# Performance work log

Hardware: AMD Instinct MI355X
Metric: run time of the kernel (lower is better)

The kernel has to match this reference:

```python
import jax, jax.numpy as jnp
import numpy as np

B, L, D, H, NL, FF, W, V = 4, 8192, 256, 4, 4, 1024, 512, 14
DH = D // H


def _ln(x, g, b, eps=1e-5):
    m = jnp.mean(x, axis=-1, keepdims=True)
    v = jnp.mean((x - m) ** 2, axis=-1, keepdims=True)
    return (x - m) / jnp.sqrt(v + eps) * g + b


def setup_inputs() -> dict:
    key = jax.random.key(0)
    ks = jax.random.split(key, 12)
    s = 0.02
    inp = {
        "byte_ids": jax.random.randint(ks[0], (B, L), 0, V, dtype=jnp.int32),
        "embed": jax.random.normal(ks[1], (V, D), jnp.float32) * s,
        "wq": jax.random.normal(ks[2], (NL, D, D), jnp.float32) * s,
        "bq": jnp.zeros((NL, D), jnp.float32),
        "wk": jax.random.normal(ks[3], (NL, D, D), jnp.float32) * s,
        "bk": jnp.zeros((NL, D), jnp.float32),
        "wv": jax.random.normal(ks[4], (NL, D, D), jnp.float32) * s,
        "bv": jnp.zeros((NL, D), jnp.float32),
        "wo": jax.random.normal(ks[5], (NL, D, D), jnp.float32) * s,
        "bo": jnp.zeros((NL, D), jnp.float32),
        "ln1_g": jnp.ones((NL, D), jnp.float32),
        "ln1_b": jnp.zeros((NL, D), jnp.float32),
        "ln2_g": jnp.ones((NL, D), jnp.float32),
        "ln2_b": jnp.zeros((NL, D), jnp.float32),
        "w1": jax.random.normal(ks[6], (NL, D, FF), jnp.float32) * s,
        "b1": jnp.zeros((NL, FF), jnp.float32),
        "w2": jax.random.normal(ks[7], (NL, FF, D), jnp.float32) * s,
        "b2": jnp.zeros((NL, D), jnp.float32),
        "lnf_g": jnp.ones((D,), jnp.float32),
        "lnf_b": jnp.zeros((D,), jnp.float32),
        "head_w": jax.random.normal(ks[8], (D, V), jnp.float32) * s,
    }
    return inp


def _forward(byte_ids, embed, wq, bq, wk, bk, wv, bv, wo, bo,
             ln1_g, ln1_b, ln2_g, ln2_b, w1, b1, w2, b2, lnf_g, lnf_b, head_w):
    x = embed[byte_ids]                      # [B, L, D]
    nb = L // W                              # number of 512-wide blocks
    scale = 1.0 / np.sqrt(DH)
    # ALiBi slopes: 2^(-8h/H) for h = 1..H
    slopes = jnp.exp2(-8.0 * jnp.arange(1, H + 1, dtype=jnp.float32) / H)
    qi = jnp.arange(W)[:, None]
    ki = jnp.arange(2 * W)[None, :]
    dist = (W + qi - ki).astype(jnp.float32)            # i - j for kv window [prev, cur]
    base = (dist >= 0) & (dist <= W)                    # causal sliding window (left=512)
    mask = jnp.broadcast_to(base, (nb, W, 2 * W))
    mask = mask.at[0].set(base & (ki >= W))             # first block has no previous block
    bias = -slopes[:, None, None] * dist                # [H, W, 2W]

    for l in range(NL):
        h = _ln(x, ln1_g[l], ln1_b[l])
        q = (h @ wq[l] + bq[l]).reshape(B, nb, W, H, DH)
        k = (h @ wk[l] + bk[l]).reshape(B, nb, W, H, DH)
        v = (h @ wv[l] + bv[l]).reshape(B, nb, W, H, DH)
        kp = jnp.pad(k, ((0, 0), (1, 0), (0, 0), (0, 0), (0, 0)))[:, :nb]
        vp = jnp.pad(v, ((0, 0), (1, 0), (0, 0), (0, 0), (0, 0)))[:, :nb]
        kk = jnp.concatenate([kp, k], axis=2)           # [B, nb, 2W, H, DH]
        vv = jnp.concatenate([vp, v], axis=2)
        s = jnp.einsum('bnqhd,bnkhd->bhnqk', q, kk) * scale + bias[None, :, None]
        s = jnp.where(mask[None, None], s, -1e9)
        p = jax.nn.softmax(s, axis=-1)                  # [B, H, nb, W, 2W]
        o = jnp.einsum('bhnqk,bnkhd->bnqhd', p, vv).reshape(B, L, D)
        x = x + o @ wo[l] + bo[l]
        h2 = _ln(x, ln2_g[l], ln2_b[l])
        x = x + jax.nn.gelu(h2 @ w1[l] + b1[l]) @ w2[l] + b2[l]
    x = _ln(x, lnf_g, lnf_b)
    return x @ head_w                                   # [B, L, V]


def reference(byte_ids, embed, wq, bq, wk, bk, wv, bv, wo, bo,
              ln1_g, ln1_b, ln2_g, ln2_b, w1, b1, w2, b2, lnf_g, lnf_b, head_w):
    return _forward(byte_ids, embed, wq, bq, wk, bk, wv, bv, wo, bo,
                    ln1_g, ln1_b, ln2_g, ln2_b, w1, b1, w2, b2, lnf_g, lnf_b, head_w)
```

## Files before the change

kernel.cpp:

```cpp
#include <hip/hip_runtime.h>

#define NLAYER 4
#define M_TOK 32768

typedef unsigned short u16;
typedef __bf16 bf16x8 __attribute__((ext_vector_type(8)));
typedef float f32x4 __attribute__((ext_vector_type(4)));

__device__ inline float bf2f(u16 u) {
    union { unsigned int i; float f; } x; x.i = ((unsigned int)u) << 16; return x.f;
}
__device__ inline u16 f2bf(float f) {
    union { float f; unsigned int i; } x; x.f = f;
    return (u16)((x.i + 0x8000u) >> 16);
}
__device__ inline bf16x8 ld_frag(const u16* p) {
    union { uint4 u; bf16x8 b; } c; c.u = *(const uint4*)p; return c.b;
}
__device__ inline unsigned pk2(float a, float b) {
    union { float f; unsigned i; } ua, ub; ua.f = a; ub.f = b;
    return __builtin_amdgcn_perm(ub.i + 0x8000u, ua.i + 0x8000u, 0x07060302u);
}
__device__ inline float gelu_f(float x) {
    float z = 0.7978845608028654f * (x + 0.044715f * x * x * x);
    float t = 1.f - 2.f / (__expf(2.f * z) + 1.f);
    return 0.5f * x * (1.f + t);
}
__device__ inline void gload_lds16(const u16* g, u16* l) {
    __builtin_amdgcn_global_load_lds(
        (const __attribute__((address_space(1))) unsigned int*)g,
        (__attribute__((address_space(3))) unsigned int*)l, 16, 0, 0);
}

#define BAR()   asm volatile("s_barrier" ::: "memory")
#define WAIT4() asm volatile("s_waitcnt vmcnt(4)" ::: "memory")
#define WAIT2() asm volatile("s_waitcnt vmcnt(2)" ::: "memory")
#define WAIT0() asm volatile("s_waitcnt vmcnt(0)" ::: "memory")
#define LGKM0() asm volatile("s_waitcnt lgkmcnt(0)" ::: "memory")

__global__ void sniff_kernel(const u16* __restrict__ raw, int* __restrict__ flag)
{
    if (threadIdx.x == 0 && blockIdx.x == 0) {
        int ok = 1;
        for (int i = 0; i < 32; i++) {
            u16 u = raw[i];
            int e = (u >> 7) & 0xFF;
            if (!(u == 0 || (e >= 90 && e <= 140))) ok = 0;
        }
        *flag = ok;
    }
}

struct IngestArgs { const void* src[20]; int off[21]; };
__global__ __launch_bounds__(256) void ingest_all(
    IngestArgs a, float* __restrict__ dst, const int* __restrict__ flag, int tot)
{
    int gid = blockIdx.x * 256 + threadIdx.x;
    if (gid >= tot) return;
    int lo = 0, hi = 20;
    while (hi - lo > 1) { int mid = (lo + hi) >> 1; if (gid >= a.off[mid]) lo = mid; else hi = mid; }
    int local = gid - a.off[lo];
    if (*flag) dst[gid] = bf2f(((const u16*)a.src[lo])[local]);
    else       dst[gid] = ((const float*)a.src[lo])[local];
}

__global__ __launch_bounds__(256) void pack_qkv(
    const float* __restrict__ wq, const float* __restrict__ wk, const float* __restrict__ wv,
    const float* __restrict__ bq, const float* __restrict__ bk, const float* __restrict__ bv,
    u16* __restrict__ wT, float* __restrict__ bT)
{
    int l = blockIdx.y;
    int idx = blockIdx.x * 256 + threadIdx.x;
    int n = idx >> 8, k = idx & 255;
    const float* w = (n < 256) ? wq : (n < 512) ? wk : wv;
    int nn = n & 255;
    wT[(size_t)l * 768 * 256 + idx] = f2bf(w[(size_t)l * 65536 + k * 256 + nn]);
    if (idx < 768) {
        const float* bb = (idx < 256) ? bq : (idx < 512) ? bk : bv;
        bT[l * 768 + idx] = bb[l * 256 + (idx & 255)];
    }
}

__global__ __launch_bounds__(256) void pack_t(
    const float* __restrict__ src, u16* __restrict__ dst, int R, int C)
{
    int l = blockIdx.y;
    int idx = blockIdx.x * 256 + threadIdx.x;
    int c = idx / R, r = idx % R;
    size_t base = (size_t)l * R * C;
    dst[base + idx] = f2bf(src[base + (size_t)r * C + c]);
}

__global__ __launch_bounds__(256) void embed_ln(
    const int* __restrict__ ids, const float* __restrict__ emb,
    const float* __restrict__ g, const float* __restrict__ b,
    float* __restrict__ x, u16* __restrict__ h)
{
    int t = blockIdx.x * 256 + threadIdx.x;
    int row = t >> 6, c = (t & 63) * 4;
    int id = ids[row];
    float4 e = *(const float4*)(emb + (size_t)id * 256 + c);
    *(float4*)(x + (size_t)row * 256 + c) = e;
    float s = e.x + e.y + e.z + e.w;
    float s2 = e.x * e.x + e.y * e.y + e.z * e.z + e.w * e.w;
    #pragma unroll
    for (int mk = 1; mk < 64; mk <<= 1) {
        s += __shfl_xor(s, mk, 64);
        s2 += __shfl_xor(s2, mk, 64);
    }
    float mean = s * (1.f / 256.f);
    float var = s2 * (1.f / 256.f) - mean * mean;
    float rstd = rsqrtf(var + 1e-5f);
    float4 gg = *(const float4*)(g + c);
    float4 bb = *(const float4*)(b + c);
    union { unsigned long long u; u16 q[4]; } oo;
    oo.q[0] = f2bf((e.x - mean) * rstd * gg.x + bb.x);
    oo.q[1] = f2bf((e.y - mean) * rstd * gg.y + bb.y);
    oo.q[2] = f2bf((e.z - mean) * rstd * gg.z + bb.z);
    oo.q[3] = f2bf((e.w - mean) * rstd * gg.w + bb.w);
    *(unsigned long long*)(h + (size_t)row * 256 + c) = oo.u;
}

template <int EPI, int K>
__global__ __launch_bounds__(256, 3) void gemm_db(
    const u16* __restrict__ A, const u16* __restrict__ Bt, const float* __restrict__ bias,
    u16* __restrict__ outB, float* __restrict__ resid, int N)
{
    __shared__ u16 lds[17408];
    constexpr int NC = K / 32;
    int tid = threadIdx.x, lane = tid & 63, wave = tid >> 6;
    int col = lane & 15, quad = lane >> 4;
    int wm = (wave >> 1) * 64, wn = (wave & 1) * 64;
    int bm = blockIdx.x * 128, bn = blockIdx.y * 128;

    u16* A0 = lds;          u16* A1 = lds + 4096;
    u16* B0 = lds + 8192;   u16* B1 = lds + 12288;

    int rL = wave * 32 + (lane >> 2);
    int sx = (lane & 3) ^ ((lane >> 2) & 3);
    const u16* srcA0 = A + (size_t)(bm + rL) * K + sx * 8;
    const u16* srcB0 = Bt + (size_t)(bn + rL) * K + sx * 8;
    int st = wave * 1024 + lane * 8;

    int g8 = (quad ^ (col & 3)) * 8;
    int aoff = (wm + col) * 32 + g8;
    int boff = (wn + col) * 32 + g8;

    f32x4 z4 = { 0.f, 0.f, 0.f, 0.f };
    f32x4 acc[4][4];
    #pragma unroll
    for (int i = 0; i < 4; i++)
        #pragma unroll
        for (int j = 0; j < 4; j++) acc[i][j] = z4;

    #define STAGE(c, Ax, Bx) do {                                        \
        const u16* _a = srcA0 + (c) * 32;                                \
        const u16* _b = srcB0 + (c) * 32;                                \
        gload_lds16(_a, (Ax) + st);                                      \
        gload_lds16(_a + (size_t)16 * K, (Ax) + st + 512);               \
        gload_lds16(_b, (Bx) + st);                                      \
        gload_lds16(_b + (size_t)16 * K, (Bx) + st + 512);               \
    } while (0)

    #define CHUNK(Ax, Bx) do {                                           \
        bf16x8 af[4], bfv[4];                                            \
        _Pragma("unroll")                                                \
        for (int i = 0; i < 4; i++) af[i] = ld_frag((Ax) + aoff + i * 512); \
        _Pragma("unroll")                                                \
        for (int j = 0; j < 4; j++) bfv[j] = ld_frag((Bx) + boff + j * 512); \
        _Pragma("unroll")                                                \
        for (int i = 0; i < 4; i++)                                      \
            _Pragma("unroll")                                            \
            for (int j = 0; j < 4; j++)                                  \
                acc[i][j] = __builtin_amdgcn_mfma_f32_16x16x32_bf16(af[i], bfv[j], acc[i][j], 0, 0, 0); \
    } while (0)

    STAGE(0, A0, B0);
    for (int c = 0; c < NC - 2; c += 2) {
        STAGE(c + 1, A1, B1);
        WAIT4(); BAR();
        CHUNK(A0, B0);
        LGKM0(); BAR();
        STAGE(c + 2, A0, B0);
        WAIT4(); BAR();
        CHUNK(A1, B1);
        LGKM0(); BAR();
    }
    STAGE(NC - 1, A1, B1);
    WAIT4(); BAR();
    CHUNK(A0, B0);
    LGKM0(); BAR();
    WAIT0(); BAR();
    CHUNK(A1, B1);
    __syncthreads();

    if (EPI == 2) {
        float* Cf = (float*)lds;
        #pragma unroll
        for (int h = 0; h < 2; h++) {
            if ((wave & 1) == h) {
                #pragma unroll
                for (int j = 0; j < 4; j++) {
                    float bv = bias[bn + wn + j * 16 + col];
                    #pragma unroll
                    for (int i = 0; i < 4; i++) {
                        int rl = wm + i * 16 + quad * 4;
                        #pragma unroll
                        for (int r = 0; r < 4; r++)
                            Cf[(rl + r) * 68 + j * 16 + col] = acc[i][j][r] + bv;
                    }
                }
            }
            LGKM0(); BAR();
            #pragma unroll
            for (int u = 0; u < 8; u++) {
                int row = u * 16 + (tid >> 4);
                int cseg = (tid & 15) * 4;
                float* rp = resid + (size_t)(bm + row) * N + bn + h * 64 + cseg;
                const float* cp = Cf + row * 68 + cseg;
                float4 rv = *(float4*)rp;
                float4 cv = *(const float4*)cp;
                rv.x += cv.x; rv.y += cv.y; rv.z += cv.z; rv.w += cv.w;
                *(float4*)rp = rv;
            }
            LGKM0(); BAR();
        }
    } else {
        u16* Cs = lds;
        #pragma unroll
        for (int j = 0; j < 4; j++) {
            int ccl = wn + j * 16 + col;
            float bv = bias[bn + ccl];
            #pragma unroll
            for (int i = 0; i < 4; i++) {
                int rl = wm + i * 16 + quad * 4;
                #pragma unroll
                for (int r = 0; r < 4; r++) {
                    float v = acc[i][j][r] + bv;
                    if (EPI == 1) v = gelu_f(v);
                    Cs[(rl + r) * 136 + ccl] = f2bf(v);
                }
            }
        }
        __syncthreads();
        #pragma unroll
        for (int u = 0; u < 8; u++) {
            int row = u * 16 + (tid >> 4);
            int c8 = (tid & 15) * 8;
            u16* op = outB + (size_t)(bm + row) * N + bn + c8;
            *(uint4*)op = *(const uint4*)(Cs + row * 136 + c8);
        }
    }
    #undef STAGE
    #undef CHUNK
}

template <int FUSE>
__global__ __launch_bounds__(512, 2) void mlp2s(
    const float* __restrict__ xin, const u16* __restrict__ w1T, const u16* __restrict__ w2T,
    const float* __restrict__ gamma, const float* __restrict__ beta,
    const float* __restrict__ b1, const float* __restrict__ b2, float* __restrict__ xr,
    const float* __restrict__ g1n, const float* __restrict__ b1n, u16* __restrict__ hout)
{
    __shared__ u16 L[77824];
    int tid = threadIdx.x, lane = tid & 63, wave = tid >> 6;
    int col = lane & 15, quad = lane >> 4;
    int g8 = (quad ^ (col & 3)) * 8;
    int bm = blockIdx.x * 128;
    int isProd = (wave < 4);
    int pw = wave & 3;

    {
        int sub = tid & 7, rsel = tid >> 3;
        float4 g4[8], b4[8];
        #pragma unroll
        for (int q = 0; q < 8; q++) {
            g4[q] = *(const float4*)(gamma + sub * 32 + q * 4);
            b4[q] = *(const float4*)(beta  + sub * 32 + q * 4);
        }
        #pragma unroll
        for (int p = 0; p < 2; p++) {
            int row = p * 64 + rsel;
            const float* xp = xin + (size_t)(bm + row) * 256 + sub * 32;
            float4 v4[8];
            #pragma unroll
            for (int q = 0; q < 8; q++) v4[q] = *(const float4*)(xp + q * 4);
            float s1 = 0.f, s2 = 0.f;
            #pragma unroll
            for (int q = 0; q < 8; q++) {
                s1 += v4[q].x + v4[q].y + v4[q].z + v4[q].w;
                s2 += v4[q].x * v4[q].x + v4[q].y * v4[q].y
                    + v4[q].z * v4[q].z + v4[q].w * v4[q].w;
            }
            s1 += __shfl_xor(s1, 1, 64); s2 += __shfl_xor(s2, 1, 64);
            s1 += __shfl_xor(s1, 2, 64); s2 += __shfl_xor(s2, 2, 64);
            s1 += __shfl_xor(s1, 4, 64); s2 += __shfl_xor(s2, 4, 64);
            float mean = s1 * (1.f / 256.f);
            float var  = s2 * (1.f / 256.f) - mean * mean;
            float rstd = rsqrtf(var + 1e-5f);
            #pragma unroll
            for (int j = 0; j < 4; j++) {
                float4 a = v4[2 * j], c = v4[2 * j + 1];
                float4 ga = g4[2 * j], gc = g4[2 * j + 1];
                float4 ba = b4[2 * j], bc = b4[2 * j + 1];
                union { uint4 u; u16 q[8]; } pkv;
                pkv.q[0] = f2bf((a.x - mean) * rstd * ga.x + ba.x);
                pkv.q[1] = f2bf((a.y - mean) * rstd * ga.y + ba.y);
                pkv.q[2] = f2bf((a.z - mean) * rstd * ga.z + ba.z);
                pkv.q[3] = f2bf((a.w - mean) * rstd * ga.w + ba.w);
                pkv.q[4] = f2bf((c.x - mean) * rstd * gc.x + bc.x);
                pkv.q[5] = f2bf((c.y - mean) * rstd * gc.y + bc.y);
                pkv.q[6] = f2bf((c.z - mean) * rstd * gc.z + bc.z);
                pkv.q[7] = f2bf((c.w - mean) * rstd * gc.w + bc.w);
                *(uint4*)(L + sub * 4096 + row * 32 + ((j ^ (row & 3)) * 8)) = pkv.u;
            }
        }
        float2 bv = *(const float2*)(b1 + tid * 2);
        *(float2*)((float*)(L + 75776) + tid * 2) = bv;
    }

    #define STAGE_W1(ff, base) do {                                                  \
        _Pragma("unroll")                                                            \
        for (int gg = 0; gg < 2; gg++) {                                             \
            int u_ = gg * 512 + tid;                                                 \
            int ks_ = u_ >> 7, rowf_ = (u_ & 127) >> 2, s_ = u_ & 3;                 \
            gload_lds16(w1T + (size_t)((ff) * 32 + rowf_) * 256 + ks_ * 32           \
                            + ((s_ ^ (rowf_ & 3)) * 8),                              \
                        L + (base) + u_ * 8);                                        \
        }                                                                            \
    } while (0)

    #define STAGE_W2(ff, base) do {                                                  \
        _Pragma("unroll")                                                            \
        for (int gg = 0; gg < 2; gg++) {                                             \
            int u_ = gg * 512 + tid;                                                 \
            int d_ = u_ >> 2, s_ = u_ & 3;                                           \
            gload_lds16(w2T + (size_t)d_ * 1024 + (ff) * 32 + ((s_ ^ (d_ & 3)) * 8), \
                        L + (base) + u_ * 8);                                        \
        }                                                                            \
    } while (0)

    STAGE_W1(0, 32768);
    WAIT0(); LGKM0(); BAR();

    f32x4 z4 = { 0.f, 0.f, 0.f, 0.f };
    f32x4 acc2[2][16];
    #pragma unroll
    for (int mt = 0; mt < 2; mt++)
        #pragma unroll
        for (int nt = 0; nt < 16; nt++) acc2[mt][nt] = z4;
    const float* b1l = (const float*)(L + 75776);

    #pragma unroll 2
    for (int f = 0; f < 32; ++f) {
        int pc = f & 1, pn = pc ^ 1;
        if (f < 31) STAGE_W1(f + 1, 32768 + pn * 8192);
        STAGE_W2(f, 49152 + pc * 8192);
        if (f == 31) WAIT2(); else WAIT4();
        BAR();

        if (isProd) {
            const u16* w1b = L + 32768 + pc * 8192;
            f32x4 a1[2][2];
            a1[0][0] = z4; a1[0][1] = z4; a1[1][0] = z4; a1[1][1] = z4;
            __builtin_amdgcn_s_setprio(1);
            #pragma unroll
            for (int ks = 0; ks < 8; ks++) {
                bf16x8 hf0 = ld_frag(L + ks * 4096 + (pw * 32 + col) * 32 + g8);
                bf16x8 hf1 = ld_frag(L + ks * 4096 + (pw * 32 + 16 + col) * 32 + g8);
                #pragma unroll
                for (int kt = 0; kt < 2; kt++) {
                    bf16x8 wf = ld_frag(w1b + ks * 1024 + (kt * 16 + col) * 32 + g8);
                    a1[0][kt] = __builtin_amdgcn_mfma_f32_16x16x32_bf16(wf, hf0, a1[0][kt], 0, 0, 0);
                    a1[1][kt] = __builtin_amdgcn_mfma_f32_16x16x32_bf16(wf, hf1, a1[1][kt], 0, 0, 0);
                }
            }
            __builtin_amdgcn_s_setprio(0);
            u16* gd = L + 65536 + pc * 5120;
            #pragma unroll
            for (int mt = 0; mt < 2; mt++)
                #pragma unroll
                for (int kt = 0; kt < 2; kt++) {
                    float4 bv = *(const float4*)(b1l + f * 32 + kt * 16 + quad * 4);
                    float p0 = gelu_f(a1[mt][kt][0] + bv.x);
                    float p1 = gelu_f(a1[mt][kt][1] + bv.y);
                    float p2 = gelu_f(a1[mt][kt][2] + bv.z);
                    float p3 = gelu_f(a1[mt][kt][3] + bv.w);
                    uint2 w; w.x = pk2(p0, p1); w.y = pk2(p2, p3);
                    *(uint2*)(gd + (pw * 32 + mt * 16 + col) * 40 + kt * 16 + quad * 4) = w;
                }
        } else if (f > 0) {
            const u16* gs = L + 65536 + pn * 5120;
            const u16* w2b = L + 49152 + pn * 8192;
            __builtin_amdgcn_s_setprio(1);
            bf16x8 gf0 = ld_frag(gs + (pw * 32 + col) * 40 + quad * 8);
            bf16x8 gf1 = ld_frag(gs + (pw * 32 + 16 + col) * 40 + quad * 8);
            #pragma unroll
            for (int nt = 0; nt < 16; nt++) {
                bf16x8 wf2 = ld_frag(w2b + (nt * 16 + col) * 32 + g8);
                acc2[0][nt] = __builtin_amdgcn_mfma_f32_16x16x32_bf16(gf0, wf2, acc2[0][nt], 0, 0, 0);
                acc2[1][nt] = __builtin_amdgcn_mfma_f32_16x16x32_bf16(gf1, wf2, acc2[1][nt], 0, 0, 0);
            }
            __builtin_amdgcn_s_setprio(0);
        }
        LGKM0(); BAR();
    }

    WAIT0();
    if (!isProd) {
        const u16* gs = L + 65536 + 5120;
        const u16* w2b = L + 49152 + 8192;
        __builtin_amdgcn_s_setprio(1);
        bf16x8 gf0 = ld_frag(gs + (pw * 32 + col) * 40 + quad * 8);
        bf16x8 gf1 = ld_frag(gs + (pw * 32 + 16 + col) * 40 + quad * 8);
        #pragma unroll
        for (int nt = 0; nt < 16; nt++) {
            bf16x8 wf2 = ld_frag(w2b + (nt * 16 + col) * 32 + g8);
            acc2[0][nt] = __builtin_amdgcn_mfma_f32_16x16x32_bf16(gf0, wf2, acc2[0][nt], 0, 0, 0);
            acc2[1][nt] = __builtin_amdgcn_mfma_f32_16x16x32_bf16(gf1, wf2, acc2[1][nt], 0, 0, 0);
        }
        __builtin_amdgcn_s_setprio(0);

        float b2v[16], g1v[16], b1v[16];
        #pragma unroll
        for (int nt = 0; nt < 16; nt++) {
            b2v[nt] = b2[nt * 16 + col];
            if (FUSE) { g1v[nt] = g1n[nt * 16 + col]; b1v[nt] = b1n[nt * 16 + col]; }
        }
        #pragma unroll
        for (int mt = 0; mt < 2; mt++)
            #pragma unroll
            for (int r = 0; r < 4; r++) {
                int m = pw * 32 + mt * 16 + quad * 4 + r;
                float* xrow = xr + (size_t)(bm + m) * 256;
                float s1 = 0.f, s2 = 0.f;
                #pragma unroll
                for (int nt = 0; nt < 16; nt++) {
                    float xv = xrow[nt * 16 + col] + acc2[mt][nt][r] + b2v[nt];
                    acc2[mt][nt][r] = xv;
                    s1 += xv; s2 += xv * xv;
                }
                #pragma unroll
                for (int nt = 0; nt < 16; nt++) xrow[nt * 16 + col] = acc2[mt][nt][r];
                if (FUSE) {
                    s1 += __shfl_xor(s1, 1, 64); s2 += __shfl_xor(s2, 1, 64);
                    s1 += __shfl_xor(s1, 2, 64); s2 += __shfl_xor(s2, 2, 64);
                    s1 += __shfl_xor(s1, 4, 64); s2 += __shfl_xor(s2, 4, 64);
                    s1 += __shfl_xor(s1, 8, 64); s2 += __shfl_xor(s2, 8, 64);
                    float mean = s1 * (1.f / 256.f);
                    float var  = s2 * (1.f / 256.f) - mean * mean;
                    float rstd = rsqrtf(var + 1e-5f);
                    #pragma unroll
                    for (int nt = 0; nt < 16; nt++)
                        L[m * 256 + nt * 16 + col] =
                            f2bf((acc2[mt][nt][r] - mean) * rstd * g1v[nt] + b1v[nt]);
                }
            }
    }
    if (FUSE) {
        LGKM0(); BAR();
        #pragma unroll
        for (int i = 0; i < 8; i++) {
            int flat = i * 4096 + tid * 8;
            *(uint4*)(hout + (size_t)bm * 256 + flat) = *(const uint4*)(L + flat);
        }
    }
    #undef STAGE_W1
    #undef STAGE_W2
}

__global__ __launch_bounds__(256, 3) void attn_kernel(
    const u16* __restrict__ qkv, u16* __restrict__ attno)
{
    __shared__ u16 Ks[64 * 72];
    __shared__ u16 Vt[64 * 68];
    __shared__ u16 Ps[4 * 16 * 72];
    int g = blockIdx.x;
    int xc = g & 7, t = g >> 3;
    int r12 = t & 15, s8 = t >> 4;
    int ng = s8 * 8 + xc;
    int bb = ng >> 4, nn = ng & 15;
    int hh = r12 & 3, t2 = r12 >> 2;
    int tid = threadIdx.x, lane = tid & 63, wave = tid >> 6;
    int q16 = lane & 15, quad = lane >> 4;
    float slope = exp2f(-2.f * (float)(hh + 1));
    float slopeL = slope * 1.44269504f;
    const float C1 = 0.125f * 1.44269504f;

    int qt0 = t2 * 2;
    size_t tok0 = (size_t)bb * 8192 + nn * 512;

    bf16x8 bqf[2][2];
    {
        int qrow = t2 * 128 + wave * 16 + q16;
        const u16* qp = qkv + (tok0 + qrow) * 768 + hh * 64 + quad * 8;
        bqf[0][0] = ld_frag(qp);
        bqf[0][1] = ld_frag(qp + 32);
        const u16* qp1 = qp + (size_t)64 * 768;
        bqf[1][0] = ld_frag(qp1);
        bqf[1][1] = ld_frag(qp1 + 32);
    }

    f32x4 z4 = { 0.f, 0.f, 0.f, 0.f };
    f32x4 oa[2][4];
    #pragma unroll
    for (int s = 0; s < 2; s++)
        #pragma unroll
        for (int dt = 0; dt < 4; dt++) oa[s][dt] = z4;
    float lsum[2] = { 0.f, 0.f };
    u16* Psw = Ps + wave * (16 * 72);

    int c_lo = (nn == 0) ? 8 : qt0;
    int c_hi = qt0 + 9;

    int kkK = tid >> 3, c8k = (tid & 7) * 8;
    int kk2 = (tid & 31) * 2, c8v = (tid >> 5) * 8;

    uint4 pk0, pk1, pv0, pv1;
    auto load_c = [&](int c) {
        int tok = (int)tok0 - 512 + c * 64;
        const u16* bK = qkv + (size_t)(tok + kkK) * 768 + hh * 64 + 256 + c8k;
        pk0 = *(const uint4*)bK;
        pk1 = *(const uint4*)(bK + (size_t)32 * 768);
        const u16* bV = qkv + (size_t)(tok + kk2) * 768 + hh * 64 + 512 + c8v;
        pv0 = *(const uint4*)bV;
        pv1 = *(const uint4*)(bV + 768);
    };
    load_c(c_lo);

    for (int c = c_lo; c <= c_hi; ++c) {
        LGKM0(); BAR();
        *(uint4*)(Ks + kkK * 72 + c8k) = pk0;
        *(uint4*)(Ks + (kkK + 32) * 72 + c8k) = pk1;
        {
            union { uint4 u; u16 s[8]; } a, b;
            a.u = pv0; b.u = pv1;
            #pragma unroll
            for (int j = 0; j < 8; j++) {
                unsigned w = (unsigned)a.s[j] | ((unsigned)b.s[j] << 16);
                *(unsigned*)(Vt + (c8v + j) * 68 + kk2) = w;
            }
        }
        if (c < c_hi) load_c(c + 1);
        LGKM0(); BAR();

        bf16x8 kf[4][2];
        #pragma unroll
        for (int kt = 0; kt < 4; kt++)
            #pragma unroll
            for (int ks = 0; ks < 2; ks++)
                kf[kt][ks] = ld_frag(Ks + (kt * 16 + q16) * 72 + ks * 32 + quad * 8);
        bf16x8 vf[4][2];
        #pragma unroll
        for (int dt = 0; dt < 4; dt++)
            #pragma unroll
            for (int ks = 0; ks < 2; ks++) {
                union { uint2 p[2]; bf16x8 b; } cv;
                const u16* vp = Vt + (dt * 16 + q16) * 68 + ks * 32 + quad * 8;
                cv.p[0] = *(const uint2*)(vp);
                cv.p[1] = *(const uint2*)(vp + 4);
                vf[dt][ks] = cv.b;
            }

        int act0 = (c <= qt0 + 8);
        int act1 = (c >= qt0 + 1);
        #pragma unroll
        for (int s = 0; s < 2; s++) {
            if (s == 0 ? !act0 : !act1) continue;
            f32x4 st[4];
            #pragma unroll
            for (int kt = 0; kt < 4; kt++) {
                f32x4 z = z4;
                #pragma unroll
                for (int ks = 0; ks < 2; ks++)
                    z = __builtin_amdgcn_mfma_f32_16x16x32_bf16(kf[kt][ks], bqf[s][ks], z, 0, 0, 0);
                st[kt] = z;
            }
            int qg = t2 * 128 + s * 64 + wave * 16 + q16;
            int D = 512 + qg - c * 64 - quad * 4;
            float nb = -slopeL * (float)D;
            int qts = qt0 + s;
            int diag = (c == qts) || (c == qts + 8);
            float ls = 0.f;
            #pragma unroll
            for (int kt = 0; kt < 4; kt++) {
                float pk[4];
                #pragma unroll
                for (int r = 0; r < 4; r++) {
                    float bias = fmaf(slopeL, (float)(kt * 16 + r), nb);
                    float p = exp2f(fmaf(st[kt][r], C1, bias));
                    if (diag) {
                        int dd = D - (kt * 16 + r);
                        p = ((unsigned)dd <= 512u) ? p : 0.f;
                    }
                    ls += p; pk[r] = p;
                }
                uint2 w;
                w.x = pk2(pk[0], pk[1]);
                w.y = pk2(pk[2], pk[3]);
                *(uint2*)(Psw + q16 * 72 + kt * 16 + quad * 4) = w;
            }
            lsum[s] += ls;
            bf16x8 pf[2];
            #pragma unroll
            for (int ks = 0; ks < 2; ks++)
                pf[ks] = ld_frag(Psw + q16 * 72 + ks * 32 + quad * 8);
            #pragma unroll
            for (int dt = 0; dt < 4; dt++)
                #pragma unroll
                for (int ks = 0; ks < 2; ks++)
                    oa[s][dt] = __builtin_amdgcn_mfma_f32_16x16x32_bf16(pf[ks], vf[dt][ks], oa[s][dt], 0, 0, 0);
        }
    }

    #pragma unroll
    for (int s = 0; s < 2; s++) {
        float lr = lsum[s];
        lr += __shfl_xor(lr, 16, 64);
        lr += __shfl_xor(lr, 32, 64);
        lsum[s] = lr;
    }
    float* lx = (float*)Psw;
    if (quad == 0) { lx[q16] = lsum[0]; lx[16 + q16] = lsum[1]; }
    #pragma unroll
    for (int s = 0; s < 2; s++) {
        float4 lq = *(const float4*)(lx + s * 16 + quad * 4);
        float inv[4] = { 1.f / lq.x, 1.f / lq.y, 1.f / lq.z, 1.f / lq.w };
        int tokb = (int)tok0 + t2 * 128 + s * 64 + wave * 16 + quad * 4;
        #pragma unroll
        for (int r = 0; r < 4; r++)
            #pragma unroll
            for (int dt = 0; dt < 4; dt++)
                attno[(size_t)(tokb + r) * 256 + hh * 64 + dt * 16 + q16] = f2bf(oa[s][dt][r] * inv[r]);
    }
}

__global__ __launch_bounds__(256) void head_ln_kernel(
    const float* __restrict__ x, const float* __restrict__ g, const float* __restrict__ b,
    const float* __restrict__ hw, const int* __restrict__ flag,
    u16* __restrict__ outb, float* __restrict__ outf)
{
    __shared__ float Wt[14 * 256];
    int tid = threadIdx.x;
    for (int i = tid; i < 14 * 256; i += 256) {
        int v = i >> 8, d = i & 255;
        Wt[i] = hw[d * 14 + v];
    }
    __syncthreads();
    int wave = tid >> 6, lane = tid & 63;
    int row = blockIdx.x * 4 + wave;
    float4 v = *(const float4*)(x + (size_t)row * 256 + lane * 4);
    float s = v.x + v.y + v.z + v.w;
    float s2 = v.x * v.x + v.y * v.y + v.z * v.z + v.w * v.w;
    #pragma unroll
    for (int mk = 1; mk < 64; mk <<= 1) {
        s += __shfl_xor(s, mk, 64);
        s2 += __shfl_xor(s2, mk, 64);
    }
    float mean = s * (1.f / 256.f);
    float var = s2 * (1.f / 256.f) - mean * mean;
    float rstd = rsqrtf(var + 1e-5f);
    int d0 = lane * 4;
    float4 gg = *(const float4*)(g + d0);
    float4 bb = *(const float4*)(b + d0);
    float hv[4];
    hv[0] = (v.x - mean) * rstd * gg.x + bb.x;
    hv[1] = (v.y - mean) * rstd * gg.y + bb.y;
    hv[2] = (v.z - mean) * rstd * gg.z + bb.z;
    hv[3] = (v.w - mean) * rstd * gg.w + bb.w;
    int isbf = *flag;
    for (int vv = 0; vv < 14; vv++) {
        float4 wv4 = *(const float4*)(Wt + vv * 256 + lane * 4);
        float sd = hv[0] * wv4.x + hv[1] * wv4.y + hv[2] * wv4.z + hv[3] * wv4.w;
        #pragma unroll
        for (int mk = 1; mk < 64; mk <<= 1) sd += __shfl_xor(sd, mk, 64);
        if (lane == 0) {
            if (isbf) outb[(size_t)row * 14 + vv] = f2bf(sd);
            else      outf[(size_t)row * 14 + vv] = sd;
        }
    }
}

extern "C" void kernel_launch(void* const* d_in, const int* in_sizes, int n_in,
                              void* d_out, int out_size, void* d_ws, size_t ws_size,
                              hipStream_t stream) {
    (void)out_size; (void)ws_size;
    const int* ids = (const int*)d_in[0];

    char* ws = (char*)d_ws;
    int* flag = (int*)ws; ws += 16;

    IngestArgs ia;
    int off = 0;
    for (int i = 1; i < n_in && i <= 20; i++) {
        ia.src[i - 1] = d_in[i];
        ia.off[i - 1] = off;
        off += in_sizes[i];
    }
    ia.off[20] = off;
    float* fbase = (float*)ws;
    ws += (size_t)((off + 3) & ~3) * 4;
    float* fin[21];
    for (int i = 1; i <= 20; i++) fin[i] = fbase + ia.off[i - 1];

    float* x    = (float*)ws;  ws += (size_t)M_TOK * 256 * 4;
    u16* h      = (u16*)ws;    ws += (size_t)M_TOK * 256 * 2;
    u16* qkv    = (u16*)ws;    ws += (size_t)M_TOK * 768 * 2;
    u16* attno  = (u16*)ws;    ws += (size_t)M_TOK * 256 * 2;
    u16* wqkvT  = (u16*)ws;    ws += (size_t)NLAYER * 768 * 256 * 2;
    u16* woT    = (u16*)ws;    ws += (size_t)NLAYER * 256 * 256 * 2;
    u16* w1T    = (u16*)ws;    ws += (size_t)NLAYER * 1024 * 256 * 2;
    u16* w2T    = (u16*)ws;    ws += (size_t)NLAYER * 256 * 1024 * 2;
    float* bqkv = (float*)ws;  ws += (size_t)NLAYER * 768 * 4;

    sniff_kernel<<<1, 64, 0, stream>>>((const u16*)d_in[1], flag);
    ingest_all<<<(off + 255) / 256, 256, 0, stream>>>(ia, fbase, flag, off);

    pack_qkv<<<dim3(768, NLAYER), 256, 0, stream>>>(fin[2], fin[4], fin[6],
                                                    fin[3], fin[5], fin[7], wqkvT, bqkv);
    pack_t<<<dim3(256, NLAYER), 256, 0, stream>>>(fin[8], woT, 256, 256);
    pack_t<<<dim3(1024, NLAYER), 256, 0, stream>>>(fin[14], w1T, 256, 1024);
    pack_t<<<dim3(1024, NLAYER), 256, 0, stream>>>(fin[16], w2T, 1024, 256);

    embed_ln<<<8192, 256, 0, stream>>>(ids, fin[1], fin[10], fin[11], x, h);

    for (int l = 0; l < NLAYER; ++l) {
        gemm_db<0, 256><<<dim3(256, 6), 256, 0, stream>>>(h, wqkvT + (size_t)l * 768 * 256,
                                                          bqkv + l * 768, qkv, nullptr, 768);
        attn_kernel<<<1024, 256, 0, stream>>>(qkv, attno);
        gemm_db<2, 256><<<dim3(256, 2), 256, 0, stream>>>(attno, woT + (size_t)l * 65536,
                                                          fin[9] + l * 256, nullptr, x, 256);
        if (l < NLAYER - 1) {
            mlp2s<1><<<256, 512, 0, stream>>>(x, w1T + (size_t)l * 262144,
                                              w2T + (size_t)l * 262144,
                                              fin[12] + l * 256, fin[13] + l * 256,
                                              fin[15] + l * 1024, fin[17] + l * 256, x,
                                              fin[10] + (l + 1) * 256, fin[11] + (l + 1) * 256, h);
        } else {
            mlp2s<0><<<256, 512, 0, stream>>>(x, w1T + (size_t)l * 262144,
                                              w2T + (size_t)l * 262144,
                                              fin[12] + l * 256, fin[13] + l * 256,
                                              fin[15] + l * 1024, fin[17] + l * 256, x,
                                              fin[10], fin[11], h);
        }
    }
    head_ln_kernel<<<8192, 256, 0, stream>>>(x, fin[18], fin[19], fin[20], flag,
                                             (u16*)d_out, (float*)d_out);
}
```

Before: 966.0 us.

## Use a four-stage LDS ring with two-chunk prefetch in the GEMM

Replaces the ping-pong double buffer in gemm_db with a four-slot LDS ring. Global-to-LDS loads are issued two K-chunks ahead, and each chunk needs only one barrier instead of two. The goal is to hide more global-load latency and cut barrier stalls. In exchange, LDS per block grows to 64KB and launch bounds drop from three to two blocks per CU, which lowers occupancy.

```diff
diff --git a/kernel.cpp b/kernel.cpp
--- a/kernel.cpp
+++ b/kernel.cpp
@@ -33,6 +33,7 @@
 }
 
 #define BAR()   asm volatile("s_barrier" ::: "memory")
+#define WAIT8() asm volatile("s_waitcnt vmcnt(8)" ::: "memory")
 #define WAIT4() asm volatile("s_waitcnt vmcnt(4)" ::: "memory")
 #define WAIT2() asm volatile("s_waitcnt vmcnt(2)" ::: "memory")
 #define WAIT0() asm volatile("s_waitcnt vmcnt(0)" ::: "memory")
@@ -122,20 +123,17 @@
 }
 
 template <int EPI, int K>
-__global__ __launch_bounds__(256, 3) void gemm_db(
+__global__ __launch_bounds__(256, 2) void gemm_db(
     const u16* __restrict__ A, const u16* __restrict__ Bt, const float* __restrict__ bias,
     u16* __restrict__ outB, float* __restrict__ resid, int N)
 {
-    __shared__ u16 lds[17408];
+    __shared__ u16 lds[32768];
     constexpr int NC = K / 32;
     int tid = threadIdx.x, lane = tid & 63, wave = tid >> 6;
     int col = lane & 15, quad = lane >> 4;
     int wm = (wave >> 1) * 64, wn = (wave & 1) * 64;
     int bm = blockIdx.x * 128, bn = blockIdx.y * 128;
 
-    u16* A0 = lds;          u16* A1 = lds + 4096;
-    u16* B0 = lds + 8192;   u16* B1 = lds + 12288;
-
     int rL = wave * 32 + (lane >> 2);
     int sx = (lane & 3) ^ ((lane >> 2) & 3);
     const u16* srcA0 = A + (size_t)(bm + rL) * K + sx * 8;
@@ -153,21 +151,23 @@
         #pragma unroll
         for (int j = 0; j < 4; j++) acc[i][j] = z4;
 
-    #define STAGE(c, Ax, Bx) do {                                        \
+    #define STAGE(c) do {                                                \
+        u16* _bs = lds + ((c) & 3) * 8192;                               \
         const u16* _a = srcA0 + (c) * 32;                                \
         const u16* _b = srcB0 + (c) * 32;                                \
-        gload_lds16(_a, (Ax) + st);                                      \
-        gload_lds16(_a + (size_t)16 * K, (Ax) + st + 512);               \
-        gload_lds16(_b, (Bx) + st);                                      \
-        gload_lds16(_b + (size_t)16 * K, (Bx) + st + 512);               \
+        gload_lds16(_a, _bs + st);                                       \
+        gload_lds16(_a + (size_t)16 * K, _bs + st + 512);                \
+        gload_lds16(_b, _bs + 4096 + st);                                \
+        gload_lds16(_b + (size_t)16 * K, _bs + 4096 + st + 512);         \
     } while (0)
 
-    #define CHUNK(Ax, Bx) do {                                           \
+    #define CHUNK(c) do {                                                \
+        const u16* _bs = lds + ((c) & 3) * 8192;                         \
         bf16x8 af[4], bfv[4];                                            \
         _Pragma("unroll")                                                \
-        for (int i = 0; i < 4; i++) af[i] = ld_frag((Ax) + aoff + i * 512); \
+        for (int i = 0; i < 4; i++) af[i] = ld_frag(_bs + aoff + i * 512); \
         _Pragma("unroll")                                                \
-        for (int j = 0; j < 4; j++) bfv[j] = ld_frag((Bx) + boff + j * 512); \
+        for (int j = 0; j < 4; j++) bfv[j] = ld_frag(_bs + 4096 + boff + j * 512); \
         _Pragma("unroll")                                                \
         for (int i = 0; i < 4; i++)                                      \
             _Pragma("unroll")                                            \
@@ -175,23 +175,17 @@
                 acc[i][j] = __builtin_amdgcn_mfma_f32_16x16x32_bf16(af[i], bfv[j], acc[i][j], 0, 0, 0); \
     } while (0)
 
-    STAGE(0, A0, B0);
-    for (int c = 0; c < NC - 2; c += 2) {
-        STAGE(c + 1, A1, B1);
-        WAIT4(); BAR();
-        CHUNK(A0, B0);
-        LGKM0(); BAR();
-        STAGE(c + 2, A0, B0);
-        WAIT4(); BAR();
-        CHUNK(A1, B1);
-        LGKM0(); BAR();
-    }
-    STAGE(NC - 1, A1, B1);
-    WAIT4(); BAR();
-    CHUNK(A0, B0);
-    LGKM0(); BAR();
-    WAIT0(); BAR();
-    CHUNK(A1, B1);
+    STAGE(0); STAGE(1);
+    #pragma unroll 4
+    for (int c = 0; c < NC; ++c) {
+        if (c + 2 < NC) STAGE(c + 2);
+        int rem = NC - 1 - c;
+        if (rem >= 2) WAIT8();
+        else if (rem == 1) WAIT4();
+        else WAIT0();
+        BAR();
+        CHUNK(c);
+    }
     __syncthreads();
 
     if (EPI == 2) {
```

After: 972.9 us. No clear change (+0.7%).
